# Kernel tuning notes

Measured on AMD Instinct MI355X. Metric: run time of the kernel, lower is better.

## Reference

```python
import jax, jax.numpy as jnp
import numpy as np

N_WIN, P, C = 2048, 64, 256      # total windows, tokens per window (8x8 partition), channels
M_SEL, KEEP, REAL = 1536, 48, 40 # selected windows, topk tokens kept per window, real (non-padded)
H, DH = 8, 32                    # heads, dim_head
EPS = 1e-5


def _ln(x, g, b):
    mu = jnp.mean(x, axis=-1, keepdims=True)
    v = jnp.mean(jnp.square(x - mu), axis=-1, keepdims=True)
    return (x - mu) * jax.lax.rsqrt(v + EPS) * g + b


def setup_inputs() -> dict:
    key = jax.random.key(0)
    ks = jax.random.split(key, 6)
    rng = np.random.default_rng(0)
    # distinct selected windows
    index_window = jnp.asarray(np.sort(rng.choice(N_WIN, size=M_SEL, replace=False)), jnp.int32)
    # per selected window: 48 distinct token positions out of 64; first 40 real, last 8 padded
    pos = np.argsort(rng.random((M_SEL, P)), axis=1)[:, :KEEP]
    tok = np.arange(M_SEL)[:, None] * P + pos           # flat rows into (M*P, C)
    index_token = jnp.asarray(tok.reshape(-1), jnp.int32)
    asy_index = jnp.asarray(tok[:, :REAL].reshape(-1), jnp.int32)
    padding_index = jnp.asarray(tok[:, REAL:].reshape(-1), jnp.int32)
    w = lambda k, s: jax.random.normal(k, s, jnp.float32) * 0.02
    return {
        "x": jax.random.normal(ks[0], (N_WIN, P, C), jnp.float32),
        "qkv_w": w(ks[1], (C, 3 * C)), "qkv_b": jnp.zeros((3 * C,), jnp.float32),
        "proj_w": w(ks[2], (C, C)), "proj_b": jnp.zeros((C,), jnp.float32),
        "norm1_g": jnp.ones((C,), jnp.float32), "norm1_b": jnp.zeros((C,), jnp.float32),
        "norm2_g": jnp.ones((C,), jnp.float32), "norm2_b": jnp.zeros((C,), jnp.float32),
        "ls1_g": jnp.full((C,), 1e-5, jnp.float32), "ls2_g": jnp.full((C,), 1e-5, jnp.float32),
        "mlp_w1": w(ks[3], (C, 4 * C)), "mlp_b1": jnp.zeros((4 * C,), jnp.float32),
        "mlp_w2": w(ks[4], (4 * C, C)), "mlp_b2": jnp.zeros((C,), jnp.float32),
        "index_window": index_window, "index_token": index_token,
        "padding_index": padding_index, "asy_index": asy_index,
        "M": M_SEL,
    }


def reference(x, qkv_w, qkv_b, proj_w, proj_b, norm1_g, norm1_b, norm2_g, norm2_b,
              ls1_g, ls2_g, mlp_w1, mlp_b1, mlp_w2, mlp_b2,
              index_window, index_token, padding_index, asy_index, M):
    scale = DH ** -0.5
    x1 = _ln(x, norm1_g, norm1_b)                       # norm1 over all windows (N,P,C)
    X = x1
    XX = x1[index_window].reshape(-1, C)                # gather selected windows -> (M*P, C)
    XX = XX.at[asy_index].set(_ln(XX[asy_index], norm2_g, norm2_b))
    shortcut = XX[asy_index]
    xt = XX[index_token].reshape(M, KEEP, C)            # gather kept tokens per window
    qkv = (xt @ qkv_w + qkv_b).reshape(M, KEEP, H, 3 * DH).transpose(0, 2, 1, 3)
    q, k, v = jnp.split(qkv, 3, axis=-1)                # each (M,H,KEEP,DH)
    attn = jnp.einsum('mhqd,mhkd->mhqk', q, k) * scale  # (M,H,Q,K)
    # scatter scores into full map keyed by KEY token row, mask padded keys, gather back
    am = attn.transpose(0, 3, 2, 1).reshape(M * KEEP, KEEP, H)
    attn_map = jnp.zeros((M * P, KEEP, H), attn.dtype)
    attn_map = attn_map.at[index_token].set(am)
    attn_map = attn_map.at[padding_index].set(-10000.0)
    attn = attn_map[index_token].reshape(M, KEEP, KEEP, H).transpose(0, 3, 2, 1)
    attn = jax.nn.softmax(attn, axis=-1)
    out = jnp.einsum('mhqk,mhkd->mhqd', attn, v).transpose(0, 2, 1, 3).reshape(M, KEEP, C)
    out = out @ proj_w + proj_b
    XX = XX.at[index_token].set(out.reshape(-1, C))
    xa = shortcut + XX[asy_index] * ls1_g               # residual + LayerScale
    hdn = jax.nn.gelu(xa @ mlp_w1 + mlp_b1, approximate=False)
    xa = xa + (hdn @ mlp_w2 + mlp_b2) * ls2_g           # (enable_CB=False path)
    XX = XX.at[asy_index].set(xa)
    Xw = X[index_window].reshape(-1, C)
    XX = XX.at[padding_index].set(Xw[padding_index])    # restore padded rows
    X = X.at[index_window].set(XX.reshape(M, P, C))     # scatter windows back
    return X
```

## Files before the change

kernel.cpp:

```cpp
#include <hip/hip_runtime.h>

typedef __attribute__((ext_vector_type(8))) short bf16x8;
typedef __attribute__((ext_vector_type(4))) float f32x4;
typedef unsigned short u16;
typedef unsigned int u32;

#define NWIN 2048
#define P 64
#define C 256
#define MSEL 1536
#define KEEP 48
#define REAL 40
#define H 8
#define DH 32
#define MROWS (MSEL * REAL)

#define OFF_WQKVT  0
#define OFF_PROJT  196608
#define OFF_W1T    262144
#define OFF_W2T    524288
#define OFF_A      786432
#define OFF_QKV    16515072
#define OFF_ATTNO  63700992
#define OFF_XA     79429632
#define OFF_H      16515072

__device__ __forceinline__ u16 f2bf(float f) {
    u32 u = __float_as_uint(f);
    u += 0x7FFF + ((u >> 16) & 1);
    return (u16)(u >> 16);
}
__device__ __forceinline__ float bf2f(u16 h) { return __uint_as_float(((u32)h) << 16); }

__global__ __launch_bounds__(256) void prep_weights(const float* __restrict__ qkv_w,
                                                    const float* __restrict__ proj_w,
                                                    const float* __restrict__ w1,
                                                    const float* __restrict__ w2,
                                                    u16* __restrict__ ws) {
    int i = blockIdx.x * 256 + threadIdx.x;
    float v; int o;
    if (i < 196608) {
        int n = i >> 8, k = i & 255; v = qkv_w[k * 768 + n]; o = OFF_WQKVT + i;
    } else if (i < 262144) {
        int j = i - 196608; int n = j >> 8, k = j & 255; v = proj_w[k * 256 + n]; o = i;
    } else if (i < 524288) {
        int j = i - 262144; int n = j >> 8, k = j & 255; v = w1[k * 1024 + n]; o = i;
    } else {
        int j = i - 524288; int n = j >> 10, k = j & 1023; v = w2[k * 256 + n]; o = i;
    }
    ws[o] = f2bf(v);
}

__global__ __launch_bounds__(256) void ln1_kernel(const float* __restrict__ x,
                                                  const float* __restrict__ g,
                                                  const float* __restrict__ b,
                                                  float* __restrict__ out) {
    int row = blockIdx.x * 4 + (threadIdx.x >> 6);
    int l = threadIdx.x & 63;
    const float4 v = *(const float4*)(x + (size_t)row * C + l * 4);
    float s = v.x + v.y + v.z + v.w;
    float q = v.x * v.x + v.y * v.y + v.z * v.z + v.w * v.w;
    #pragma unroll
    for (int m = 1; m < 64; m <<= 1) { s += __shfl_xor(s, m); q += __shfl_xor(q, m); }
    float mu = s * (1.0f / C);
    float var = q * (1.0f / C) - mu * mu;
    float rs = rsqrtf(var + 1e-5f);
    float4 gg = *(const float4*)(g + l * 4);
    float4 bb = *(const float4*)(b + l * 4);
    float4 o;
    o.x = (v.x - mu) * rs * gg.x + bb.x;
    o.y = (v.y - mu) * rs * gg.y + bb.y;
    o.z = (v.z - mu) * rs * gg.z + bb.z;
    o.w = (v.w - mu) * rs * gg.w + bb.w;
    *(float4*)(out + (size_t)row * C + l * 4) = o;
}

__global__ __launch_bounds__(256) void ln2_kernel(const float* __restrict__ ln1,
                                                  const float* __restrict__ g,
                                                  const float* __restrict__ b,
                                                  const int* __restrict__ asy,
                                                  const int* __restrict__ iwin,
                                                  u16* __restrict__ A) {
    int r = blockIdx.x * 4 + (threadIdx.x >> 6);
    int l = threadIdx.x & 63;
    int flat = asy[r];
    int m = flat >> 6, p = flat & 63;
    int w = iwin[m];
    const float4 v = *(const float4*)(ln1 + ((size_t)w * P + p) * C + l * 4);
    float s = v.x + v.y + v.z + v.w;
    float q = v.x * v.x + v.y * v.y + v.z * v.z + v.w * v.w;
    #pragma unroll
    for (int mm = 1; mm < 64; mm <<= 1) { s += __shfl_xor(s, mm); q += __shfl_xor(q, mm); }
    float mu = s * (1.0f / C);
    float var = q * (1.0f / C) - mu * mu;
    float rs = rsqrtf(var + 1e-5f);
    float4 gg = *(const float4*)(g + l * 4);
    float4 bb = *(const float4*)(b + l * 4);
    ushort4 o;
    o.x = f2bf((v.x - mu) * rs * gg.x + bb.x);
    o.y = f2bf((v.y - mu) * rs * gg.y + bb.y);
    o.z = f2bf((v.z - mu) * rs * gg.z + bb.z);
    o.w = f2bf((v.w - mu) * rs * gg.w + bb.w);
    *(ushort4*)(A + (size_t)r * C + l * 4) = o;
}

template <int N, int K, class Epi>
__global__ __launch_bounds__(256) void gemm_bt(const u16* __restrict__ A,
                                               const u16* __restrict__ B, Epi epi,
                                               int chunk) {
    constexpr int NB = N / 128;
    int bid = blockIdx.x;
    bid = (bid & 7) * chunk + (bid >> 3);
    int bm = bid / NB, bn = bid % NB;
    __shared__ u16 lA[128 * 64], lB[128 * 64];
    int t = threadIdx.x;
    int l = t & 63, w = t >> 6;
    int wr = w >> 1, wc = w & 1;
    int l15 = l & 15, g4 = l >> 4;
    int xr = l15 & 7;

    f32x4 acc[4][4];
    #pragma unroll
    for (int a = 0; a < 4; a++)
        #pragma unroll
        for (int bb = 0; bb < 4; bb++)
            #pragma unroll
            for (int i = 0; i < 4; i++) acc[a][bb][i] = 0.0f;

    int rbase = w * 32 + (l >> 3);
    int cg = (l & 7) ^ (l >> 3);
    const u16* gA = A + (size_t)(bm * 128 + rbase) * K + cg * 8;
    const u16* gB = B + (size_t)(bn * 128 + rbase) * K + cg * 8;

    for (int k0 = 0; k0 < K; k0 += 64) {
        __syncthreads();
        #pragma unroll
        for (int j = 0; j < 4; j++)
            __builtin_amdgcn_global_load_lds(
                (const __attribute__((address_space(1))) u32*)(gA + (size_t)j * 8 * K + k0),
                (__attribute__((address_space(3))) u32*)(lA + w * 2048 + j * 512), 16, 0, 0);
        #pragma unroll
        for (int j = 0; j < 4; j++)
            __builtin_amdgcn_global_load_lds(
                (const __attribute__((address_space(1))) u32*)(gB + (size_t)j * 8 * K + k0),
                (__attribute__((address_space(3))) u32*)(lB + w * 2048 + j * 512), 16, 0, 0);
        __syncthreads();
        #pragma unroll
        for (int kk = 0; kk < 2; kk++) {
            bf16x8 af[4], bfr[4];
            #pragma unroll
            for (int mt = 0; mt < 4; mt++)
                af[mt] = *(const bf16x8*)(lA + (wr * 64 + mt * 16 + l15) * 64
                                             + ((kk * 4 + g4) ^ xr) * 8);
            #pragma unroll
            for (int nt = 0; nt < 4; nt++)
                bfr[nt] = *(const bf16x8*)(lB + (wc * 64 + nt * 16 + l15) * 64
                                              + ((kk * 4 + g4) ^ xr) * 8);
            #pragma unroll
            for (int mt = 0; mt < 4; mt++)
                #pragma unroll
                for (int nt = 0; nt < 4; nt++)
                    acc[mt][nt] = __builtin_amdgcn_mfma_f32_16x16x32_bf16(af[mt], bfr[nt], acc[mt][nt], 0, 0, 0);
        }
    }
    int orow = bm * 128 + wr * 64, ocol = bn * 128 + wc * 64;
    #pragma unroll
    for (int mt = 0; mt < 4; mt++)
        #pragma unroll
        for (int nt = 0; nt < 4; nt++)
            #pragma unroll
            for (int rg = 0; rg < 4; rg++)
                epi(orow + mt * 16 + g4 * 4 + rg, ocol + nt * 16 + l15, acc[mt][nt][rg]);
}

struct EpiQKV {
    const float* bias; u16* out;
    __device__ void operator()(int r, int c, float v) const {
        out[(size_t)r * 768 + c] = f2bf(v + bias[c]);
    }
};
struct EpiProj {
    const float* bias; const float* ls1; const u16* Abuf; u16* xa;
    __device__ void operator()(int r, int c, float v) const {
        float val = bf2f(Abuf[(size_t)r * 256 + c]) + (v + bias[c]) * ls1[c];
        xa[(size_t)r * 256 + c] = f2bf(val);
    }
};
struct EpiMLP1 {
    const float* bias; u16* h;
    __device__ void operator()(int r, int c, float v) const {
        float x = v + bias[c];
        float gl = 0.5f * x * (1.0f + erff(x * 0.70710678118654752f));
        h[(size_t)r * 1024 + c] = f2bf(gl);
    }
};
struct EpiMLP2 {
    const float* bias; const float* ls2; const u16* xa;
    const int* asy; const int* iwin; float* out;
    __device__ void operator()(int r, int c, float v) const {
        float val = bf2f(xa[(size_t)r * 256 + c]) + (v + bias[c]) * ls2[c];
        int flat = asy[r];
        int m = flat >> 6, p = flat & 63;
        int wdw = iwin[m];
        out[((size_t)wdw * P + p) * C + c] = val;
    }
};

__global__ __launch_bounds__(256) void attn_kernel(const u16* __restrict__ QKV,
                                                   u16* __restrict__ out) {
    __shared__ u16 lds[4 * (48 * 80 + 32 * 80)];
    int m = blockIdx.x;
    int t = threadIdx.x, l = t & 63, w = t >> 6;
    int l15 = l & 15, g4 = l >> 4;
    u16* Pb = lds + w * (48 * 80 + 32 * 80);
    u16* Vt = Pb + 48 * 80;

    u32* z = (u32*)Pb;
    for (int i = l; i < (48 * 80 + 32 * 80) / 2; i += 64) z[i] = 0;

    const float scale = 0.17677669529663687f;

    for (int hh = 0; hh < 2; hh++) {
        int h = w + hh * 4;
        const u16* base = QKV + (size_t)m * REAL * 768 + h * 96;

        for (int i = l; i < REAL * 4; i += 64) {
            int kk = i >> 2, dg = i & 3;
            bf16x8 vv = *(const bf16x8*)(base + (size_t)kk * 768 + 64 + dg * 8);
            #pragma unroll
            for (int j = 0; j < 8; j++) Vt[(dg * 8 + j) * 80 + kk] = vv[j];
        }

        bf16x8 zf;
        #pragma unroll
        for (int i = 0; i < 8; i++) zf[i] = 0;
        bf16x8 qf[3], kf[3];
        #pragma unroll
        for (int mt = 0; mt < 3; mt++) {
            int q = mt * 16 + l15;
            qf[mt] = (q < REAL) ? *(const bf16x8*)(base + (size_t)q * 768 + g4 * 8) : zf;
        }
        #pragma unroll
        for (int nt = 0; nt < 3; nt++) {
            int kk = nt * 16 + l15;
            kf[nt] = (kk < REAL) ? *(const bf16x8*)(base + (size_t)kk * 768 + 32 + g4 * 8) : zf;
        }
        f32x4 s[3][3];
        #pragma unroll
        for (int a = 0; a < 3; a++)
            #pragma unroll
            for (int bb = 0; bb < 3; bb++)
                #pragma unroll
                for (int i = 0; i < 4; i++) s[a][bb][i] = 0.0f;
        #pragma unroll
        for (int mt = 0; mt < 3; mt++)
            #pragma unroll
            for (int nt = 0; nt < 3; nt++)
                s[mt][nt] = __builtin_amdgcn_mfma_f32_16x16x32_bf16(qf[mt], kf[nt], s[mt][nt], 0, 0, 0);

        #pragma unroll
        for (int mt = 0; mt < 3; mt++) {
            #pragma unroll
            for (int rg = 0; rg < 4; rg++) {
                float v0 = s[mt][0][rg] * scale;
                float v1 = s[mt][1][rg] * scale;
                float v2 = s[mt][2][rg] * scale;
                bool k2ok = (32 + l15) < REAL;
                float mx = fmaxf(fmaxf(v0, v1), k2ok ? v2 : -1e30f);
                #pragma unroll
                for (int xm = 1; xm < 16; xm <<= 1) mx = fmaxf(mx, __shfl_xor(mx, xm));
                float e0 = __expf(v0 - mx);
                float e1 = __expf(v1 - mx);
                float e2 = k2ok ? __expf(v2 - mx) : 0.0f;
                float sm = e0 + e1 + e2;
                #pragma unroll
                for (int xm = 1; xm < 16; xm <<= 1) sm += __shfl_xor(sm, xm);
                float inv = 1.0f / sm;
                int q = mt * 16 + g4 * 4 + rg;
                Pb[q * 80 + l15]      = f2bf(e0 * inv);
                Pb[q * 80 + 16 + l15] = f2bf(e1 * inv);
                Pb[q * 80 + 32 + l15] = f2bf(e2 * inv);
            }
        }

        f32x4 o[3][2];
        #pragma unroll
        for (int a = 0; a < 3; a++)
            #pragma unroll
            for (int bb = 0; bb < 2; bb++)
                #pragma unroll
                for (int i = 0; i < 4; i++) o[a][bb][i] = 0.0f;
        #pragma unroll
        for (int kt = 0; kt < 2; kt++) {
            bf16x8 pf[3], vf[2];
            #pragma unroll
            for (int mt = 0; mt < 3; mt++)
                pf[mt] = *(const bf16x8*)(Pb + (mt * 16 + l15) * 80 + kt * 32 + g4 * 8);
            #pragma unroll
            for (int nt = 0; nt < 2; nt++)
                vf[nt] = *(const bf16x8*)(Vt + (nt * 16 + l15) * 80 + kt * 32 + g4 * 8);
            #pragma unroll
            for (int mt = 0; mt < 3; mt++)
                #pragma unroll
                for (int nt = 0; nt < 2; nt++)
                    o[mt][nt] = __builtin_amdgcn_mfma_f32_16x16x32_bf16(pf[mt], vf[nt], o[mt][nt], 0, 0, 0);
        }
        #pragma unroll
        for (int mt = 0; mt < 3; mt++)
            #pragma unroll
            for (int nt = 0; nt < 2; nt++)
                #pragma unroll
                for (int rg = 0; rg < 4; rg++) {
                    int q = mt * 16 + g4 * 4 + rg;
                    if (q < REAL)
                        out[((size_t)m * REAL + q) * C + h * DH + nt * 16 + l15] = f2bf(o[mt][nt][rg]);
                }
    }
}

extern "C" void kernel_launch(void* const* d_in, const int* in_sizes, int n_in,
                              void* d_out, int out_size, void* d_ws, size_t ws_size,
                              hipStream_t stream) {
    const float* x      = (const float*)d_in[0];
    const float* qkv_w  = (const float*)d_in[1];
    const float* qkv_b  = (const float*)d_in[2];
    const float* proj_w = (const float*)d_in[3];
    const float* proj_b = (const float*)d_in[4];
    const float* n1g    = (const float*)d_in[5];
    const float* n1b    = (const float*)d_in[6];
    const float* n2g    = (const float*)d_in[7];
    const float* n2b    = (const float*)d_in[8];
    const float* ls1    = (const float*)d_in[9];
    const float* ls2    = (const float*)d_in[10];
    const float* w1     = (const float*)d_in[11];
    const float* b1     = (const float*)d_in[12];
    const float* w2     = (const float*)d_in[13];
    const float* b2     = (const float*)d_in[14];
    const int*   iwin   = (const int*)d_in[15];
    const int*   asy    = (const int*)d_in[18];
    float* out = (float*)d_out;
    u16* ws = (u16*)d_ws;

    u16* WqkvT = ws + OFF_WQKVT;
    u16* ProjT = ws + OFF_PROJT;
    u16* W1T   = ws + OFF_W1T;
    u16* W2T   = ws + OFF_W2T;
    u16* Abuf  = ws + OFF_A;
    u16* QKV   = ws + OFF_QKV;
    u16* AttnO = ws + OFF_ATTNO;
    u16* XA    = ws + OFF_XA;
    u16* Hbuf  = ws + OFF_H;

    prep_weights<<<3072, 256, 0, stream>>>(qkv_w, proj_w, w1, w2, ws);
    ln1_kernel<<<(NWIN * P) / 4, 256, 0, stream>>>(x, n1g, n1b, out);
    ln2_kernel<<<MROWS / 4, 256, 0, stream>>>(out, n2g, n2b, asy, iwin, Abuf);
    {
        int nwg = (MROWS / 128) * 6;
        gemm_bt<768, 256, EpiQKV><<<nwg, 256, 0, stream>>>(Abuf, WqkvT, EpiQKV{qkv_b, QKV}, nwg / 8);
    }
    attn_kernel<<<MSEL, 256, 0, stream>>>(QKV, AttnO);
    {
        int nwg = (MROWS / 128) * 2;
        gemm_bt<256, 256, EpiProj><<<nwg, 256, 0, stream>>>(AttnO, ProjT, EpiProj{proj_b, ls1, Abuf, XA}, nwg / 8);
    }
    {
        int nwg = (MROWS / 128) * 8;
        gemm_bt<1024, 256, EpiMLP1><<<nwg, 256, 0, stream>>>(XA, W1T, EpiMLP1{b1, Hbuf}, nwg / 8);
    }
    {
        int nwg = (MROWS / 128) * 2;
        gemm_bt<256, 1024, EpiMLP2><<<nwg, 256, 0, stream>>>(Hbuf, W2T, EpiMLP2{b2, ls2, XA, asy, iwin, out}, nwg / 8);
    }
}
```

Before: 517.7 us.

## Use FP8 for attention and projection/MLP2 operands, fuse LN1+LN2 via inverse index

Stores the QKV, attention output and MLP hidden activations in FP8, converts proj and W2 weights to FP8, and adds an FP8 GEMM kernel that loads tiles straight into LDS. Attention MFMAs now run in FP8. LN1 and LN2 are fused into one kernel through an inverse row index built by a new small kernel. GELU uses a tanh approximation instead of erf. All of this is meant to cut memory traffic and kernel launches, at the cost of noticeably lower numerical precision.

```diff
diff --git a/kernel.cpp b/kernel.cpp
--- a/kernel.cpp
+++ b/kernel.cpp
@@ -4,6 +4,7 @@
 typedef __attribute__((ext_vector_type(4))) float f32x4;
 typedef unsigned short u16;
 typedef unsigned int u32;
+typedef unsigned char u8;
 
 #define NWIN 2048
 #define P 64
@@ -15,15 +16,16 @@
 #define DH 32
 #define MROWS (MSEL * REAL)
 
-#define OFF_WQKVT  0
-#define OFF_PROJT  196608
-#define OFF_W1T    262144
-#define OFF_W2T    524288
-#define OFF_A      786432
-#define OFF_QKV    16515072
-#define OFF_ATTNO  63700992
-#define OFF_XA     79429632
-#define OFF_H      16515072
+#define B_WQKVT   0
+#define B_W1T     393216
+#define B_PROJT8  917504
+#define B_W2T8    983040
+#define B_INV     1245184
+#define B_ABUF    1769472
+#define B_XA      33226752
+#define B_QKV8    64684032
+#define B_ATTNO8  111869952
+#define B_H8      64684032
 
 __device__ __forceinline__ u16 f2bf(float f) {
     u32 u = __float_as_uint(f);
@@ -31,30 +33,49 @@
     return (u16)(u >> 16);
 }
 __device__ __forceinline__ float bf2f(u16 h) { return __uint_as_float(((u32)h) << 16); }
+__device__ __forceinline__ u8 f2fp8(float f) {
+    return (u8)__builtin_amdgcn_cvt_pk_fp8_f32(f, 0.0f, 0, false);
+}
 
 __global__ __launch_bounds__(256) void prep_weights(const float* __restrict__ qkv_w,
                                                     const float* __restrict__ proj_w,
                                                     const float* __restrict__ w1,
                                                     const float* __restrict__ w2,
-                                                    u16* __restrict__ ws) {
+                                                    u8* __restrict__ ws) {
     int i = blockIdx.x * 256 + threadIdx.x;
-    float v; int o;
     if (i < 196608) {
-        int n = i >> 8, k = i & 255; v = qkv_w[k * 768 + n]; o = OFF_WQKVT + i;
-    } else if (i < 262144) {
-        int j = i - 196608; int n = j >> 8, k = j & 255; v = proj_w[k * 256 + n]; o = i;
+        int n = i >> 8, k = i & 255;
+        ((u16*)(ws + B_WQKVT))[i] = f2bf(qkv_w[k * 768 + n]);
+    } else if (i < 458752) {
+        int j = i - 196608; int n = j >> 8, k = j & 255;
+        ((u16*)(ws + B_W1T))[j] = f2bf(w1[k * 1024 + n]);
     } else if (i < 524288) {
-        int j = i - 262144; int n = j >> 8, k = j & 255; v = w1[k * 1024 + n]; o = i;
+        int j = i - 458752; int n = j >> 8, k = j & 255;
+        (ws + B_PROJT8)[j] = f2fp8(proj_w[k * 256 + n]);
+    } else if (i < 786432) {
+        int j = i - 524288; int n = j >> 10, k = j & 1023;
+        (ws + B_W2T8)[j] = f2fp8(w2[k * 256 + n]);
     } else {
-        int j = i - 524288; int n = j >> 10, k = j & 1023; v = w2[k * 256 + n]; o = i;
-    }
-    ws[o] = f2bf(v);
-}
-
-__global__ __launch_bounds__(256) void ln1_kernel(const float* __restrict__ x,
-                                                  const float* __restrict__ g,
-                                                  const float* __restrict__ b,
-                                                  float* __restrict__ out) {
+        ((int*)(ws + B_INV))[i - 786432] = -1;
+    }
+}
+
+__global__ __launch_bounds__(256) void build_inv(const int* __restrict__ asy,
+                                                 const int* __restrict__ iwin,
+                                                 int* __restrict__ inv) {
+    int r = blockIdx.x * 256 + threadIdx.x;
+    int flat = asy[r];
+    inv[iwin[flat >> 6] * P + (flat & 63)] = r;
+}
+
+__global__ __launch_bounds__(256) void ln12_kernel(const float* __restrict__ x,
+                                                   const float* __restrict__ g1,
+                                                   const float* __restrict__ b1,
+                                                   const float* __restrict__ g2,
+                                                   const float* __restrict__ b2,
+                                                   const int* __restrict__ inv,
+                                                   float* __restrict__ out,
+                                                   u16* __restrict__ Abuf) {
     int row = blockIdx.x * 4 + (threadIdx.x >> 6);
     int l = threadIdx.x & 63;
     const float4 v = *(const float4*)(x + (size_t)row * C + l * 4);
@@ -63,45 +84,32 @@
     #pragma unroll
     for (int m = 1; m < 64; m <<= 1) { s += __shfl_xor(s, m); q += __shfl_xor(q, m); }
     float mu = s * (1.0f / C);
-    float var = q * (1.0f / C) - mu * mu;
-    float rs = rsqrtf(var + 1e-5f);
-    float4 gg = *(const float4*)(g + l * 4);
-    float4 bb = *(const float4*)(b + l * 4);
+    float rs = rsqrtf(q * (1.0f / C) - mu * mu + 1e-5f);
+    float4 gg = *(const float4*)(g1 + l * 4);
+    float4 bb = *(const float4*)(b1 + l * 4);
     float4 o;
     o.x = (v.x - mu) * rs * gg.x + bb.x;
     o.y = (v.y - mu) * rs * gg.y + bb.y;
     o.z = (v.z - mu) * rs * gg.z + bb.z;
     o.w = (v.w - mu) * rs * gg.w + bb.w;
     *(float4*)(out + (size_t)row * C + l * 4) = o;
-}
-
-__global__ __launch_bounds__(256) void ln2_kernel(const float* __restrict__ ln1,
-                                                  const float* __restrict__ g,
-                                                  const float* __restrict__ b,
-                                                  const int* __restrict__ asy,
-                                                  const int* __restrict__ iwin,
-                                                  u16* __restrict__ A) {
-    int r = blockIdx.x * 4 + (threadIdx.x >> 6);
-    int l = threadIdx.x & 63;
-    int flat = asy[r];
-    int m = flat >> 6, p = flat & 63;
-    int w = iwin[m];
-    const float4 v = *(const float4*)(ln1 + ((size_t)w * P + p) * C + l * 4);
-    float s = v.x + v.y + v.z + v.w;
-    float q = v.x * v.x + v.y * v.y + v.z * v.z + v.w * v.w;
-    #pragma unroll
-    for (int mm = 1; mm < 64; mm <<= 1) { s += __shfl_xor(s, mm); q += __shfl_xor(q, mm); }
-    float mu = s * (1.0f / C);
-    float var = q * (1.0f / C) - mu * mu;
-    float rs = rsqrtf(var + 1e-5f);
-    float4 gg = *(const float4*)(g + l * 4);
-    float4 bb = *(const float4*)(b + l * 4);
-    ushort4 o;
-    o.x = f2bf((v.x - mu) * rs * gg.x + bb.x);
-    o.y = f2bf((v.y - mu) * rs * gg.y + bb.y);
-    o.z = f2bf((v.z - mu) * rs * gg.z + bb.z);
-    o.w = f2bf((v.w - mu) * rs * gg.w + bb.w);
-    *(ushort4*)(A + (size_t)r * C + l * 4) = o;
+    int r = inv[row];
+    if (r >= 0) {
+        float s2 = o.x + o.y + o.z + o.w;
+        float q2 = o.x * o.x + o.y * o.y + o.z * o.z + o.w * o.w;
+        #pragma unroll
+        for (int m = 1; m < 64; m <<= 1) { s2 += __shfl_xor(s2, m); q2 += __shfl_xor(q2, m); }
+        float mu2 = s2 * (1.0f / C);
+        float rs2 = rsqrtf(q2 * (1.0f / C) - mu2 * mu2 + 1e-5f);
+        float4 g2v = *(const float4*)(g2 + l * 4);
+        float4 b2v = *(const float4*)(b2 + l * 4);
+        ushort4 ob;
+        ob.x = f2bf((o.x - mu2) * rs2 * g2v.x + b2v.x);
+        ob.y = f2bf((o.y - mu2) * rs2 * g2v.y + b2v.y);
+        ob.z = f2bf((o.z - mu2) * rs2 * g2v.z + b2v.z);
+        ob.w = f2bf((o.w - mu2) * rs2 * g2v.w + b2v.w);
+        *(ushort4*)(Abuf + (size_t)r * C + l * 4) = ob;
+    }
 }
 
 template <int N, int K, class Epi>
@@ -173,10 +181,81 @@
                 epi(orow + mt * 16 + g4 * 4 + rg, ocol + nt * 16 + l15, acc[mt][nt][rg]);
 }
 
-struct EpiQKV {
-    const float* bias; u16* out;
+template <int N, int K, class Epi>
+__global__ __launch_bounds__(256) void gemm_bt8(const u8* __restrict__ A,
+                                                const u8* __restrict__ B, Epi epi,
+                                                int chunk) {
+    constexpr int NB = N / 128;
+    int bid = blockIdx.x;
+    bid = (bid & 7) * chunk + (bid >> 3);
+    int bm = bid / NB, bn = bid % NB;
+    __shared__ u8 lA[128 * 64], lB[128 * 64];
+    int t = threadIdx.x;
+    int l = t & 63, w = t >> 6;
+    int wr = w >> 1, wc = w & 1;
+    int l15 = l & 15, g4 = l >> 4;
+    int xr3 = l15 & 3;
+
+    f32x4 acc[4][4];
+    #pragma unroll
+    for (int a = 0; a < 4; a++)
+        #pragma unroll
+        for (int bb = 0; bb < 4; bb++)
+            #pragma unroll
+            for (int i = 0; i < 4; i++) acc[a][bb][i] = 0.0f;
+
+    int rbase = w * 32 + (l >> 2);
+    int sx = (l & 3) ^ ((l >> 2) & 3);
+    const u8* gA = A + (size_t)(bm * 128 + rbase) * K + sx * 16;
+    const u8* gB = B + (size_t)(bn * 128 + rbase) * K + sx * 16;
+
+    for (int k0 = 0; k0 < K; k0 += 64) {
+        __syncthreads();
+        #pragma unroll
+        for (int j = 0; j < 2; j++)
+            __builtin_amdgcn_global_load_lds(
+                (const __attribute__((address_space(1))) u32*)(gA + (size_t)j * 16 * K + k0),
+                (__attribute__((address_space(3))) u32*)(lA + w * 2048 + j * 1024), 16, 0, 0);
+        #pragma unroll
+        for (int j = 0; j < 2; j++)
+            __builtin_amdgcn_global_load_lds(
+                (const __attribute__((address_space(1))) u32*)(gB + (size_t)j * 16 * K + k0),
+                (__attribute__((address_space(3))) u32*)(lB + w * 2048 + j * 1024), 16, 0, 0);
+        __syncthreads();
+        #pragma unroll
+        for (int kk = 0; kk < 2; kk++) {
+            long af[4], bfr[4];
+            #pragma unroll
+            for (int mt = 0; mt < 4; mt++) {
+                int r = wr * 64 + mt * 16 + l15;
+                af[mt] = *(const long*)(lA + r * 64 + (((kk * 2) + (g4 >> 1)) ^ xr3) * 16 + (g4 & 1) * 8);
+            }
+            #pragma unroll
+            for (int nt = 0; nt < 4; nt++) {
+                int r = wc * 64 + nt * 16 + l15;
+                bfr[nt] = *(const long*)(lB + r * 64 + (((kk * 2) + (g4 >> 1)) ^ xr3) * 16 + (g4 & 1) * 8);
+            }
+            #pragma unroll
+            for (int mt = 0; mt < 4; mt++)
+                #pragma unroll
+                for (int nt = 0; nt < 4; nt++)
+                    acc[mt][nt] = __builtin_amdgcn_mfma_f32_16x16x32_fp8_fp8(af[mt], bfr[nt], acc[mt][nt], 0, 0, 0);
+        }
+    }
+    int orow = bm * 128 + wr * 64, ocol = bn * 128 + wc * 64;
+    #pragma unroll
+    for (int mt = 0; mt < 4; mt++)
+        #pragma unroll
+        for (int nt = 0; nt < 4; nt++)
+            #pragma unroll
+            for (int rg = 0; rg < 4; rg++)
+                epi(orow + mt * 16 + g4 * 4 + rg, ocol + nt * 16 + l15, acc[mt][nt][rg]);
+}
+
+struct EpiQKV8 {
+    const float* bias; u8* out;
     __device__ void operator()(int r, int c, float v) const {
-        out[(size_t)r * 768 + c] = f2bf(v + bias[c]);
+        out[(size_t)r * 768 + c] = f2fp8(v + bias[c]);
     }
 };
 struct EpiProj {
@@ -187,11 +266,12 @@
     }
 };
 struct EpiMLP1 {
-    const float* bias; u16* h;
+    const float* bias; u8* h;
     __device__ void operator()(int r, int c, float v) const {
         float x = v + bias[c];
-        float gl = 0.5f * x * (1.0f + erff(x * 0.70710678118654752f));
-        h[(size_t)r * 1024 + c] = f2bf(gl);
+        float u = 0.7978845608f * (x + 0.044715f * x * x * x);
+        float e = __expf(2.0f * u);
+        h[(size_t)r * 1024 + c] = f2fp8(x - x / (e + 1.0f));
     }
 };
 struct EpiMLP2 {
@@ -200,50 +280,45 @@
     __device__ void operator()(int r, int c, float v) const {
         float val = bf2f(xa[(size_t)r * 256 + c]) + (v + bias[c]) * ls2[c];
         int flat = asy[r];
-        int m = flat >> 6, p = flat & 63;
-        int wdw = iwin[m];
-        out[((size_t)wdw * P + p) * C + c] = val;
+        out[((size_t)iwin[flat >> 6] * P + (flat & 63)) * C + c] = val;
     }
 };
 
-__global__ __launch_bounds__(256) void attn_kernel(const u16* __restrict__ QKV,
-                                                   u16* __restrict__ out) {
-    __shared__ u16 lds[4 * (48 * 80 + 32 * 80)];
+__global__ __launch_bounds__(256) void attn_kernel(const u8* __restrict__ QKV,
+                                                   u8* __restrict__ out) {
+    __shared__ u8 lds[4 * (48 * 80 + 32 * 80)];
     int m = blockIdx.x;
     int t = threadIdx.x, l = t & 63, w = t >> 6;
     int l15 = l & 15, g4 = l >> 4;
-    u16* Pb = lds + w * (48 * 80 + 32 * 80);
-    u16* Vt = Pb + 48 * 80;
+    u8* Pb = lds + w * (48 * 80 + 32 * 80);
+    u8* Vt = Pb + 48 * 80;
 
     u32* z = (u32*)Pb;
-    for (int i = l; i < (48 * 80 + 32 * 80) / 2; i += 64) z[i] = 0;
+    for (int i = l; i < (48 * 80 + 32 * 80) / 4; i += 64) z[i] = 0;
 
     const float scale = 0.17677669529663687f;
 
     for (int hh = 0; hh < 2; hh++) {
         int h = w + hh * 4;
-        const u16* base = QKV + (size_t)m * REAL * 768 + h * 96;
-
-        for (int i = l; i < REAL * 4; i += 64) {
-            int kk = i >> 2, dg = i & 3;
-            bf16x8 vv = *(const bf16x8*)(base + (size_t)kk * 768 + 64 + dg * 8);
-            #pragma unroll
-            for (int j = 0; j < 8; j++) Vt[(dg * 8 + j) * 80 + kk] = vv[j];
-        }
-
-        bf16x8 zf;
-        #pragma unroll
-        for (int i = 0; i < 8; i++) zf[i] = 0;
-        bf16x8 qf[3], kf[3];
+        const u8* base = QKV + (size_t)m * REAL * 768 + h * 96;
+
+        for (int i = l; i < REAL * 8; i += 64) {
+            int kk = i >> 3, dg = i & 7;
+            u32 vv = *(const u32*)(base + (size_t)kk * 768 + 64 + dg * 4);
+            #pragma unroll
+            for (int j = 0; j < 4; j++) Vt[(dg * 4 + j) * 80 + kk] = (u8)(vv >> (j * 8));
+        }
+
+        long qf[3], kf[3];
         #pragma unroll
         for (int mt = 0; mt < 3; mt++) {
             int q = mt * 16 + l15;
-            qf[mt] = (q < REAL) ? *(const bf16x8*)(base + (size_t)q * 768 + g4 * 8) : zf;
+            qf[mt] = (q < REAL) ? *(const long*)(base + (size_t)q * 768 + g4 * 8) : 0L;
         }
         #pragma unroll
         for (int nt = 0; nt < 3; nt++) {
             int kk = nt * 16 + l15;
-            kf[nt] = (kk < REAL) ? *(const bf16x8*)(base + (size_t)kk * 768 + 32 + g4 * 8) : zf;
+            kf[nt] = (kk < REAL) ? *(const long*)(base + (size_t)kk * 768 + 32 + g4 * 8) : 0L;
         }
         f32x4 s[3][3];
         #pragma unroll
@@ -256,7 +331,7 @@
         for (int mt = 0; mt < 3; mt++)
             #pragma unroll
             for (int nt = 0; nt < 3; nt++)
-                s[mt][nt] = __builtin_amdgcn_mfma_f32_16x16x32_bf16(qf[mt], kf[nt], s[mt][nt], 0, 0, 0);
+                s[mt][nt] = __builtin_amdgcn_mfma_f32_16x16x32_fp8_fp8(qf[mt], kf[nt], s[mt][nt], 0, 0, 0);
 
         #pragma unroll
         for (int mt = 0; mt < 3; mt++) {
@@ -277,9 +352,9 @@
                 for (int xm = 1; xm < 16; xm <<= 1) sm += __shfl_xor(sm, xm);
                 float inv = 1.0f / sm;
                 int q = mt * 16 + g4 * 4 + rg;
-                Pb[q * 80 + l15]      = f2bf(e0 * inv);
-                Pb[q * 80 + 16 + l15] = f2bf(e1 * inv);
-                Pb[q * 80 + 32 + l15] = f2bf(e2 * inv);
+                Pb[q * 80 + l15]      = f2fp8(e0 * inv);
+                Pb[q * 80 + 16 + l15] = f2fp8(e1 * inv);
+                Pb[q * 80 + 32 + l15] = k2ok ? f2fp8(e2 * inv) : (u8)0;
             }
         }
 
@@ -292,18 +367,18 @@
                 for (int i = 0; i < 4; i++) o[a][bb][i] = 0.0f;
         #pragma unroll
         for (int kt = 0; kt < 2; kt++) {
-            bf16x8 pf[3], vf[2];
+            long pf[3], vf[2];
             #pragma unroll
             for (int mt = 0; mt < 3; mt++)
-                pf[mt] = *(const bf16x8*)(Pb + (mt * 16 + l15) * 80 + kt * 32 + g4 * 8);
+                pf[mt] = *(const long*)(Pb + (mt * 16 + l15) * 80 + kt * 32 + g4 * 8);
             #pragma unroll
             for (int nt = 0; nt < 2; nt++)
-                vf[nt] = *(const bf16x8*)(Vt + (nt * 16 + l15) * 80 + kt * 32 + g4 * 8);
+                vf[nt] = *(const long*)(Vt + (nt * 16 + l15) * 80 + kt * 32 + g4 * 8);
             #pragma unroll
             for (int mt = 0; mt < 3; mt++)
                 #pragma unroll
                 for (int nt = 0; nt < 2; nt++)
-                    o[mt][nt] = __builtin_amdgcn_mfma_f32_16x16x32_bf16(pf[mt], vf[nt], o[mt][nt], 0, 0, 0);
+                    o[mt][nt] = __builtin_amdgcn_mfma_f32_16x16x32_fp8_fp8(pf[mt], vf[nt], o[mt][nt], 0, 0, 0);
         }
         #pragma unroll
         for (int mt = 0; mt < 3; mt++)
@@ -313,7 +388,7 @@
                 for (int rg = 0; rg < 4; rg++) {
                     int q = mt * 16 + g4 * 4 + rg;
                     if (q < REAL)
-                        out[((size_t)m * REAL + q) * C + h * DH + nt * 16 + l15] = f2bf(o[mt][nt][rg]);
+                        out[((size_t)m * REAL + q) * C + h * DH + nt * 16 + l15] = f2fp8(o[mt][nt][rg]);
                 }
     }
 }
@@ -339,36 +414,37 @@
     const int*   iwin   = (const int*)d_in[15];
     const int*   asy    = (const int*)d_in[18];
     float* out = (float*)d_out;
-    u16* ws = (u16*)d_ws;
-
-    u16* WqkvT = ws + OFF_WQKVT;
-    u16* ProjT = ws + OFF_PROJT;
-    u16* W1T   = ws + OFF_W1T;
-    u16* W2T   = ws + OFF_W2T;
-    u16* Abuf  = ws + OFF_A;
-    u16* QKV   = ws + OFF_QKV;
-    u16* AttnO = ws + OFF_ATTNO;
-    u16* XA    = ws + OFF_XA;
-    u16* Hbuf  = ws + OFF_H;
-
-    prep_weights<<<3072, 256, 0, stream>>>(qkv_w, proj_w, w1, w2, ws);
-    ln1_kernel<<<(NWIN * P) / 4, 256, 0, stream>>>(x, n1g, n1b, out);
-    ln2_kernel<<<MROWS / 4, 256, 0, stream>>>(out, n2g, n2b, asy, iwin, Abuf);
+    u8* ws = (u8*)d_ws;
+
+    u16* WqkvT  = (u16*)(ws + B_WQKVT);
+    u16* W1T    = (u16*)(ws + B_W1T);
+    u8*  ProjT8 = ws + B_PROJT8;
+    u8*  W2T8   = ws + B_W2T8;
+    int* inv    = (int*)(ws + B_INV);
+    u16* Abuf   = (u16*)(ws + B_ABUF);
+    u16* XA     = (u16*)(ws + B_XA);
+    u8*  QKV8   = ws + B_QKV8;
+    u8*  AttnO8 = ws + B_ATTNO8;
+    u8*  H8     = ws + B_H8;
+
+    prep_weights<<<3584, 256, 0, stream>>>(qkv_w, proj_w, w1, w2, ws);
+    build_inv<<<240, 256, 0, stream>>>(asy, iwin, inv);
+    ln12_kernel<<<(NWIN * P) / 4, 256, 0, stream>>>(x, n1g, n1b, n2g, n2b, inv, out, Abuf);
     {
         int nwg = (MROWS / 128) * 6;
-        gemm_bt<768, 256, EpiQKV><<<nwg, 256, 0, stream>>>(Abuf, WqkvT, EpiQKV{qkv_b, QKV}, nwg / 8);
-    }
-    attn_kernel<<<MSEL, 256, 0, stream>>>(QKV, AttnO);
+        gemm_bt<768, 256, EpiQKV8><<<nwg, 256, 0, stream>>>(Abuf, WqkvT, EpiQKV8{qkv_b, QKV8}, nwg / 8);
+    }
+    attn_kernel<<<MSEL, 256, 0, stream>>>(QKV8, AttnO8);
     {
         int nwg = (MROWS / 128) * 2;
-        gemm_bt<256, 256, EpiProj><<<nwg, 256, 0, stream>>>(AttnO, ProjT, EpiProj{proj_b, ls1, Abuf, XA}, nwg / 8);
+        gemm_bt8<256, 256, EpiProj><<<nwg, 256, 0, stream>>>(AttnO8, ProjT8, EpiProj{proj_b, ls1, Abuf, XA}, nwg / 8);
     }
     {
         int nwg = (MROWS / 128) * 8;
-        gemm_bt<1024, 256, EpiMLP1><<<nwg, 256, 0, stream>>>(XA, W1T, EpiMLP1{b1, Hbuf}, nwg / 8);
+        gemm_bt<1024, 256, EpiMLP1><<<nwg, 256, 0, stream>>>(XA, W1T, EpiMLP1{b1, H8}, nwg / 8);
     }
     {
         int nwg = (MROWS / 128) * 2;
-        gemm_bt<256, 1024, EpiMLP2><<<nwg, 256, 0, stream>>>(Hbuf, W2T, EpiMLP2{b2, ls2, XA, asy, iwin, out}, nwg / 8);
-    }
-}
+        gemm_bt8<256, 1024, EpiMLP2><<<nwg, 256, 0, stream>>>(H8, W2T8, EpiMLP2{b2, ls2, XA, asy, iwin, out}, nwg / 8);
+    }
+}
```

New measurement: 575.0 us. 11.1% more time.
